# Kernel optimization log

Measured on AMD Instinct MI355X. Metric: run time of the kernel, lower is better.

The kernel has to match this reference:

```python
import jax, jax.numpy as jnp
import numpy as np

T, B, H, K, V, O, VS, DM = 128, 256, 128, 64, 128, 512, 3, 32


def _ln(x):
    m = jnp.mean(x, -1, keepdims=True)
    v = jnp.var(x, -1, keepdims=True)
    return (x - m) / jnp.sqrt(v + 1e-5)


def setup_inputs() -> dict:
    key = jax.random.key(0)
    ks = jax.random.split(key, 16)
    n = lambda k, shape, std=0.02: jax.random.normal(k, shape, jnp.float32) * std
    return {
        "obs": jax.random.randint(ks[0], (T, B), 0, O),
        "vel": jax.random.normal(ks[1], (T, B, VS), jnp.float32),
        "exploration": jax.random.uniform(ks[2], (T, B), dtype=jnp.float32),
        "hidden_init": n(ks[3], (1, H), 0.5),
        "embed_W": n(ks[4], (O, H)),
        "vel_W": n(ks[5], (H, VS)), "vel_b": jnp.zeros((H,), jnp.float32),
        "hyp_W1": n(ks[6], (DM, VS)), "hyp_b1": jnp.zeros((DM,), jnp.float32),
        "hyp_W2": n(ks[7], (H * H, DM), 0.001), "hyp_b2": jnp.zeros((H * H,), jnp.float32),
        "gate_W": n(ks[8], (H, 2 * H)), "gate_b": jnp.zeros((H,), jnp.float32),
        "pred_W": n(ks[9], (O, H)), "pred_b": jnp.zeros((O,), jnp.float32),
        "mem_W1": n(ks[10], (200, 3)), "mem_b1": jnp.zeros((200,), jnp.float32),
        "mem_W2": n(ks[11], (1, 200)), "mem_b2": jnp.zeros((1,), jnp.float32),
        "Wqk": n(ks[12], (K, H)), "Wv": n(ks[13], (V, H)),
    }


def reference(obs, vel, exploration, hidden_init, embed_W, vel_W, vel_b,
              hyp_W1, hyp_b1, hyp_W2, hyp_b2, gate_W, gate_b, pred_W, pred_b,
              mem_W1, mem_b1, mem_W2, mem_b2, Wqk, Wv):
    i_to_h_all = embed_W[obs]                                       # [T,B,H]
    vel_emb_all = jnp.einsum('tbv,hv->tbh', vel, vel_W) + vel_b      # [T,B,H]
    hyp_h = jax.nn.silu(jnp.einsum('tbv,dv->tbd', vel, hyp_W1) + hyp_b1)  # [T,B,DM]
    h0 = jnp.tanh(jnp.tile(hidden_init, (B, 1)))                     # [B,H]
    keys0 = jnp.zeros((T, B, K), jnp.float32)
    vals0 = jnp.zeros((T, B, V), jnp.float32)
    probs0 = jnp.zeros((T, B), jnp.float32)
    scale = 1.0 / np.sqrt(K).astype(np.float32)

    def step(carry, xs):
        hidden, keys, vals, probs = carry
        i, i_to_h, hyp_t, vemb_t, expl_t = xs
        # hypernet-generated per-sample transition matrix + path integration
        Tm = (hyp_t @ hyp_W2.T + hyp_b2).reshape(B, H, H)
        pi = jnp.einsum('bij,bj->bi', Tm, hidden) + vemb_t
        pi_pred = _ln(jnp.tanh(pi))
        # external-memory dot-product attention over stored (key, value) slots
        q = pi_pred @ Wqk.T                                          # [B,K]
        scores = jnp.einsum('bk,tbk->tb', q, keys) * scale           # [T,B]
        valid = jnp.arange(T)[:, None] < i
        attn = jax.nn.softmax(jnp.where(valid, scores, -1e9), axis=0)
        has_mem = (i > 0).astype(jnp.float32)
        mem_ret = jnp.einsum('tb,tbv->bv', attn * probs, vals) * has_mem
        mem = _ln(mem_ret)
        # sigmoid-gated RNN update between generative (pi) and input paths
        gate = jax.nn.sigmoid(jnp.concatenate([pi, i_to_h], -1) @ gate_W.T + gate_b)
        hidden_new = jnp.tanh(gate * pi + (1.0 - gate) * i_to_h)
        # EM model predicts from the retrieved + normalized memory
        logits = mem @ pred_W.T + pred_b                             # [B,O]
        # write decision MLP on [max inner prod, normalized position, exploration]
        max_ip = jnp.max(jnp.where(valid, scores, -1e9), axis=0) * has_mem
        pos = jnp.full((B,), 1.0, jnp.float32) * (i.astype(jnp.float32) / T)
        feat = jnp.stack([max_ip, pos, expl_t], -1)                  # [B,3]
        h1 = jax.nn.leaky_relu(feat @ mem_W1.T + mem_b1, 0.1)
        p_write = jax.nn.sigmoid(h1 @ mem_W2.T + mem_b2)[:, 0]
        keys = keys.at[i].set(hidden_new @ Wqk.T)
        vals = vals.at[i].set(hidden_new @ Wv.T)
        probs = probs.at[i].set(p_write)
        return (hidden_new, keys, vals, probs), (logits, hidden_new, pi, gate)

    xs = (jnp.arange(T), i_to_h_all, hyp_h, vel_emb_all, exploration)
    _, (logits, inf_h, gen, gating) = jax.lax.scan(step, (h0, keys0, vals0, probs0), xs)
    preds = jax.nn.softmax(logits, axis=-1)
    return preds, logits, inf_h, gen, gating
```

## Files before the change

kernel.cpp:

```cpp
#include <hip/hip_runtime.h>

#ifndef __has_builtin
#define __has_builtin(x) 0
#endif

#define DEV static __device__ __forceinline__

#define TT 128
#define BB 256
#define HH 128
#define KK 64
#define VV 128
#define OO 512
#define JBLK 132
#define KEXT (JBLK*32)

static const size_t PRED_OFF  = 0;
static const size_t LOGIT_OFF = (size_t)TT*BB*OO;
static const size_t INFH_OFF  = LOGIT_OFF + (size_t)TT*BB*OO;
static const size_t GEN_OFF   = INFH_OFF + (size_t)TT*BB*HH;
static const size_t GATE_OFF  = GEN_OFF + (size_t)TT*BB*HH;

DEV unsigned short f2bf(float x){
  unsigned int u = __float_as_uint(x);
  u = (u + 0x7fffu + ((u >> 16) & 1u)) >> 16;
  return (unsigned short)u;
}
DEV float bf2f(unsigned short v){ return __uint_as_float(((unsigned int)v) << 16); }

#if __has_builtin(__builtin_amdgcn_cvt_pk_f32_fp8)
#define FP8_FAST_DEC 1
typedef float floatx2 __attribute__((ext_vector_type(2)));
#endif

DEV float dec8_sw(unsigned int b){
  unsigned int s = b >> 7, e = (b >> 3) & 15u, m = b & 7u;
  float v = e ? ldexpf((float)(8u + m), (int)e - 10) : ldexpf((float)m, -9);
  return s ? -v : v;
}

DEV unsigned char enc8_sw(float x){
  unsigned int u = __float_as_uint(x);
  unsigned int s = (u >> 24) & 0x80u;
  int e = (int)((u >> 23) & 0xffu) - 127;
  unsigned int m = u & 0x7fffffu;
  if (((u >> 23) & 0xffu) == 0) return (unsigned char)s;
  if (e < -10) return (unsigned char)s;
  if (e >= -6) {
    unsigned int mant = m >> 20, rem = m & 0xfffffu;
    if (rem > 0x80000u || (rem == 0x80000u && (mant & 1u))) mant++;
    unsigned int ee = (unsigned int)(e + 7);
    if (mant == 8u) { mant = 0u; ee++; }
    if (ee >= 15u) return (unsigned char)(s | 0x7Eu);
    return (unsigned char)(s | (ee << 3) | mant);
  }
  unsigned int full = 0x800000u | m;
  int sh = 20 + (-6 - e);
  unsigned int mant = full >> sh;
  unsigned int rem  = full & ((1u << sh) - 1u);
  unsigned int halfv = 1u << (sh - 1);
  if (rem > halfv || (rem == halfv && (mant & 1u))) mant++;
  if (mant >= 8u) return (unsigned char)(s | (1u << 3));
  return (unsigned char)(s | mant);
}

DEV unsigned char enc8(float v){
#if __has_builtin(__builtin_amdgcn_cvt_pk_fp8_f32)
  int r = __builtin_amdgcn_cvt_pk_fp8_f32(v, v, 0, false);
  return (unsigned char)(r & 0xff);
#else
  return enc8_sw(v);
#endif
}

__global__ __launch_bounds__(256) void k_pack(const float* __restrict__ hW2,
                                              const float* __restrict__ hb2,
                                              unsigned char* __restrict__ w2p){
  int D = blockIdx.x * 256 + threadIdx.x;
  if (D >= KEXT * HH / 4) return;
  int bq = D & 3;
  int ig = (D >> 2) & 31;
  int h  = (D >> 7) & 1;
  int n  = (D >> 8) & 3;
  int j  = D >> 10;
  int i  = ig * 4 + n;
  unsigned int outw = 0;
  for (int c = 0; c < 4; ++c) {
    int bb = bq * 4 + c;
    int k = j * 32 + h * 16 + bb;
    float v;
    if (j < 128) v = hW2[((size_t)i * HH + j) * 32 + (k & 31)];
    else         v = hb2[(size_t)i * HH + (k - 4096)];
    v *= 1024.0f;
    outw |= ((unsigned int)enc8(v)) << (8 * c);
  }
  ((unsigned int*)w2p)[D] = outw;
}

struct ScanSmem {
  unsigned short gw[128 * 258];
  float part[16 * 128];
  float x[256];
  float pi[128];
  float i2h[128];
  float h[128];
  float hyp[32];
  float velWs[HH * 3];
  float velbs[HH];
  float hypW1s[32 * 3];
  float hypb1s[32];
  float gbs[HH];
  float vel3[4];
};

__global__ __launch_bounds__(512) void k_scan(
    const int* __restrict__ obs, const float* __restrict__ vel,
    const float* __restrict__ hinit, const float* __restrict__ embW,
    const float* __restrict__ velW, const float* __restrict__ velb,
    const float* __restrict__ hW1, const float* __restrict__ hb1,
    const float* __restrict__ gW, const float* __restrict__ gb,
    const unsigned char* __restrict__ w2p,
    float* __restrict__ out)
{
  extern __shared__ char smemraw[];
  ScanSmem* sm = (ScanSmem*)smemraw;
  const int tid = threadIdx.x;
  const int b = blockIdx.x;

  for (int idx = tid; idx < 128 * 256; idx += 512) {
    int i = idx >> 8, c = idx & 255;
    sm->gw[i * 258 + c] = f2bf(gW[i * 256 + c]);
  }
  for (int idx = tid; idx < HH * 3; idx += 512) sm->velWs[idx] = velW[idx];
  for (int idx = tid; idx < HH; idx += 512) { sm->velbs[idx] = velb[idx]; sm->gbs[idx] = gb[idx]; }
  for (int idx = tid; idx < 96; idx += 512) sm->hypW1s[idx] = hW1[idx];
  if (tid < 32) sm->hypb1s[tid] = hb1[tid];
  if (tid < 128) sm->h[tid] = tanhf(hinit[tid]);
  __syncthreads();

  const int ig = tid & 31;
  const int ks = tid >> 5;
  const int jbeg = ks * 8 + (ks < 4 ? ks : 4);
  const int jend = jbeg + 8 + (ks < 4 ? 1 : 0);

  for (int t = 0; t < TT; ++t) {
    if (tid < 3) sm->vel3[tid] = vel[((size_t)t * BB + b) * 3 + tid];
    if (tid >= 128 && tid < 256) {
      int j = tid - 128;
      sm->i2h[j] = embW[(size_t)obs[t * BB + b] * HH + j];
    }
    __syncthreads();
    if (tid < 32) {
      float a = sm->vel3[0] * sm->hypW1s[tid * 3] + sm->vel3[1] * sm->hypW1s[tid * 3 + 1]
              + sm->vel3[2] * sm->hypW1s[tid * 3 + 2] + sm->hypb1s[tid];
      sm->hyp[tid] = a / (1.0f + __expf(-a));
    }
    __syncthreads();

    float hypr[32];
    #pragma unroll
    for (int d = 0; d < 32; d += 4) {
      float4 q4 = *(const float4*)&sm->hyp[d];
      hypr[d] = q4.x; hypr[d + 1] = q4.y; hypr[d + 2] = q4.z; hypr[d + 3] = q4.w;
    }

    float acc0 = 0.f, acc1 = 0.f, acc2 = 0.f, acc3 = 0.f;
    for (int j = jbeg; j < jend; ++j) {
      float uj[32];
      if (j < 128) {
        float hj = sm->h[j];
        #pragma unroll
        for (int d = 0; d < 32; ++d) uj[d] = hj * hypr[d];
      } else {
        int base = (j - 128) * 32;
        #pragma unroll
        for (int d = 0; d < 32; d += 4) {
          float4 q4 = *(const float4*)&sm->h[base + d];
          uj[d] = q4.x; uj[d + 1] = q4.y; uj[d + 2] = q4.z; uj[d + 3] = q4.w;
        }
      }
      const unsigned char* pj = w2p + (size_t)j * 4096 + (size_t)ig * 16;
      #pragma unroll
      for (int n = 0; n < 4; ++n) {
        uint4 wa = *(const uint4*)(pj + (n * 2 + 0) * 512);
        uint4 wb = *(const uint4*)(pj + (n * 2 + 1) * 512);
        const unsigned int* wpa = (const unsigned int*)&wa;
        const unsigned int* wpb = (const unsigned int*)&wb;
        float s = 0.f;
        #pragma unroll
        for (int q = 0; q < 4; ++q) {
          unsigned int ww = wpa[q];
#if defined(FP8_FAST_DEC)
          floatx2 lo = __builtin_amdgcn_cvt_pk_f32_fp8((int)ww, false);
          floatx2 hi = __builtin_amdgcn_cvt_pk_f32_fp8((int)ww, true);
          s += lo[0]*uj[q*4+0] + lo[1]*uj[q*4+1] + hi[0]*uj[q*4+2] + hi[1]*uj[q*4+3];
#else
          s += dec8_sw(ww & 0xffu)        * uj[q*4+0];
          s += dec8_sw((ww >> 8) & 0xffu) * uj[q*4+1];
          s += dec8_sw((ww >> 16) & 0xffu)* uj[q*4+2];
          s += dec8_sw((ww >> 24) & 0xffu)* uj[q*4+3];
#endif
        }
        #pragma unroll
        for (int q = 0; q < 4; ++q) {
          unsigned int ww = wpb[q];
#if defined(FP8_FAST_DEC)
          floatx2 lo = __builtin_amdgcn_cvt_pk_f32_fp8((int)ww, false);
          floatx2 hi = __builtin_amdgcn_cvt_pk_f32_fp8((int)ww, true);
          s += lo[0]*uj[16+q*4+0] + lo[1]*uj[16+q*4+1] + hi[0]*uj[16+q*4+2] + hi[1]*uj[16+q*4+3];
#else
          s += dec8_sw(ww & 0xffu)        * uj[16+q*4+0];
          s += dec8_sw((ww >> 8) & 0xffu) * uj[16+q*4+1];
          s += dec8_sw((ww >> 16) & 0xffu)* uj[16+q*4+2];
          s += dec8_sw((ww >> 24) & 0xffu)* uj[16+q*4+3];
#endif
        }
        if (n == 0) acc0 += s; else if (n == 1) acc1 += s; else if (n == 2) acc2 += s; else acc3 += s;
      }
    }
    *(float4*)&sm->part[ks * 128 + ig * 4] = make_float4(acc0, acc1, acc2, acc3);
    __syncthreads();

    if (tid < 128) {
      float s = 0.f;
      #pragma unroll
      for (int q = 0; q < 16; ++q) s += sm->part[q * 128 + tid];
      s *= (1.0f / 1024.0f);
      s += sm->vel3[0] * sm->velWs[tid * 3] + sm->vel3[1] * sm->velWs[tid * 3 + 1]
         + sm->vel3[2] * sm->velWs[tid * 3 + 2] + sm->velbs[tid];
      sm->pi[tid] = s;
      sm->x[tid] = s;
      out[GEN_OFF + ((size_t)t * BB + b) * HH + tid] = s;
    } else if (tid < 256) {
      sm->x[tid] = sm->i2h[tid - 128];
    }
    __syncthreads();

    {
      int i = tid & 127, kq = tid >> 7;
      const unsigned short* gr = &sm->gw[i * 258 + kq * 64];
      const float* xr = &sm->x[kq * 64];
      float s = 0.f;
      #pragma unroll 16
      for (int c = 0; c < 64; ++c) s += bf2f(gr[c]) * xr[c];
      sm->part[kq * 128 + i] = s;
    }
    __syncthreads();

    if (tid < 128) {
      float z = sm->part[tid] + sm->part[128 + tid] + sm->part[256 + tid] + sm->part[384 + tid] + sm->gbs[tid];
      float g = 1.0f / (1.0f + __expf(-z));
      float hn = tanhf(g * sm->pi[tid] + (1.0f - g) * sm->i2h[tid]);
      out[GATE_OFF + ((size_t)t * BB + b) * HH + tid] = g;
      out[INFH_OFF + ((size_t)t * BB + b) * HH + tid] = hn;
      sm->h[tid] = hn;
    }
    __syncthreads();
  }
}

struct QkvSmem {
  float wqk[64 * 132];
  float wv[128 * 132];
  float pp[132];
  float hh[132];
  float red[4];
  float stats[2];
};

__global__ __launch_bounds__(256) void k_qkv(const float* __restrict__ out,
    const float* __restrict__ Wqk, const float* __restrict__ Wv,
    float* __restrict__ qbuf, unsigned short* __restrict__ keysBF,
    unsigned short* __restrict__ valsBF)
{
  extern __shared__ char smemraw[];
  QkvSmem* sm = (QkvSmem*)smemraw;
  const int tid = threadIdx.x, b = blockIdx.x;

  for (int idx = tid; idx < 64 * 128; idx += 256) { int o = idx >> 7, j = idx & 127; sm->wqk[o * 132 + j] = Wqk[idx]; }
  for (int idx = tid; idx < 128 * 128; idx += 256) { int o = idx >> 7, j = idx & 127; sm->wv[o * 132 + j] = Wv[idx]; }
  __syncthreads();

  for (int t = 0; t < TT; ++t) {
    if (tid < 128) {
      size_t base = ((size_t)t * BB + b) * HH + tid;
      sm->hh[tid] = out[INFH_OFF + base];
      sm->pp[tid] = tanhf(out[GEN_OFF + base]);
    }
    __syncthreads();
    if (tid < 128) {
      float v = sm->pp[tid];
      float s1 = v, s2 = v * v;
      #pragma unroll
      for (int off = 32; off; off >>= 1) { s1 += __shfl_down(s1, off); s2 += __shfl_down(s2, off); }
      if ((tid & 63) == 0) { sm->red[tid >> 6] = s1; sm->red[2 + (tid >> 6)] = s2; }
    }
    __syncthreads();
    if (tid == 0) {
      float s1 = sm->red[0] + sm->red[1], s2 = sm->red[2] + sm->red[3];
      float m = s1 * (1.0f / 128.0f);
      float var = s2 * (1.0f / 128.0f) - m * m;
      sm->stats[0] = m; sm->stats[1] = rsqrtf(var + 1e-5f);
    }
    __syncthreads();
    if (tid < 128) sm->pp[tid] = (sm->pp[tid] - sm->stats[0]) * sm->stats[1];
    __syncthreads();
    {
      int o = tid;
      if (o < 64) {
        const float* wr = &sm->wqk[o * 132];
        float s = 0.f;
        #pragma unroll 8
        for (int j = 0; j < 128; j += 4) {
          float4 xv = *(const float4*)&sm->pp[j];
          float4 w4 = *(const float4*)&wr[j];
          s += xv.x * w4.x + xv.y * w4.y + xv.z * w4.z + xv.w * w4.w;
        }
        qbuf[((size_t)t * BB + b) * KK + o] = s;
      } else if (o < 128) {
        int kk = o - 64;
        const float* wr = &sm->wqk[kk * 132];
        float s = 0.f;
        #pragma unroll 8
        for (int j = 0; j < 128; j += 4) {
          float4 xv = *(const float4*)&sm->hh[j];
          float4 w4 = *(const float4*)&wr[j];
          s += xv.x * w4.x + xv.y * w4.y + xv.z * w4.z + xv.w * w4.w;
        }
        keysBF[((size_t)t * BB + b) * KK + kk] = f2bf(s);
      } else {
        int vv = o - 128;
        const float* wr = &sm->wv[vv * 132];
        float s = 0.f;
        #pragma unroll 8
        for (int j = 0; j < 128; j += 4) {
          float4 xv = *(const float4*)&sm->hh[j];
          float4 w4 = *(const float4*)&wr[j];
          s += xv.x * w4.x + xv.y * w4.y + xv.z * w4.z + xv.w * w4.w;
        }
        valsBF[((size_t)t * BB + b) * VV + vv] = f2bf(s);
      }
    }
    __syncthreads();
  }
}

struct ScoresSmem { float q[128 * 68]; };

__global__ __launch_bounds__(128) void k_scores(const float* __restrict__ qbuf,
    const unsigned short* __restrict__ keysBF, const float* __restrict__ expl,
    const float* __restrict__ mW1, const float* __restrict__ mb1,
    const float* __restrict__ mW2, const float* __restrict__ mb2,
    float* __restrict__ Sg, float* __restrict__ probs)
{
  extern __shared__ char smemraw[];
  ScoresSmem* sm = (ScoresSmem*)smemraw;
  const int tid = threadIdx.x, b = blockIdx.x;

  for (int idx = tid; idx < 128 * 64; idx += 128) {
    int tq = idx >> 6, c = idx & 63;
    sm->q[tq * 68 + c] = qbuf[((size_t)tq * BB + b) * KK + c];
  }
  float kreg[64];
  {
    const uint4* kp = (const uint4*)&keysBF[((size_t)tid * BB + b) * KK];
    #pragma unroll
    for (int qq = 0; qq < 8; ++qq) {
      uint4 kv = kp[qq];
      const unsigned short* ku = (const unsigned short*)&kv;
      #pragma unroll
      for (int c = 0; c < 8; ++c) kreg[qq * 8 + c] = bf2f(ku[c]);
    }
  }
  __syncthreads();

  float* srow = &Sg[(size_t)b * TT * TT];
  for (int tq = 0; tq < TT; ++tq) {
    float s = 0.f;
    #pragma unroll
    for (int c = 0; c < 64; c += 4) {
      float4 qv = *(const float4*)&sm->q[tq * 68 + c];
      s += qv.x * kreg[c] + qv.y * kreg[c + 1] + qv.z * kreg[c + 2] + qv.w * kreg[c + 3];
    }
    srow[(size_t)tq * TT + tid] = s * 0.125f;
  }
  __syncthreads();

  {
    int tq = tid;
    const float* r = &srow[(size_t)tq * TT];
    float mx = -3.0e38f;
    for (int tk = 0; tk < tq; ++tk) mx = fmaxf(mx, r[tk]);
    float f0 = (tq > 0) ? mx : 0.0f;
    float f1 = (float)tq * (1.0f / 128.0f);
    float f2 = expl[(size_t)tq * BB + b];
    float a = 0.f;
    for (int u = 0; u < 200; ++u) {
      float h1 = mW1[u * 3] * f0 + mW1[u * 3 + 1] * f1 + mW1[u * 3 + 2] * f2 + mb1[u];
      h1 = (h1 > 0.f) ? h1 : 0.1f * h1;
      a += mW2[u] * h1;
    }
    float p = 1.0f / (1.0f + __expf(-(a + mb2[0])));
    probs[(size_t)b * TT + tq] = p;
  }
}

struct AttnSmem {
  float w[32 * 132];
  float mem[32 * 132];
  float pw[128 * 132];
};

__global__ __launch_bounds__(256) void k_attn(const float* __restrict__ Sg,
    const float* __restrict__ probs, const unsigned short* __restrict__ valsBF,
    const float* __restrict__ pW, const float* __restrict__ pb,
    float* __restrict__ out)
{
  extern __shared__ char smemraw[];
  AttnSmem* sm = (AttnSmem*)smemraw;
  const int tid = threadIdx.x;
  const int t = blockIdx.x >> 3, g = blockIdx.x & 7;
  const int bloc = tid >> 3, s8 = tid & 7;
  const int b = g * 32 + bloc;

  float acc[16];
  #pragma unroll
  for (int c = 0; c < 16; ++c) acc[c] = 0.f;

  float inv = 0.f;
  if (t > 0) {
    const float* srow = &Sg[((size_t)b * TT + t) * TT];
    float mx = -3.0e38f;
    for (int tk = s8; tk < t; tk += 8) mx = fmaxf(mx, srow[tk]);
    #pragma unroll
    for (int off = 4; off; off >>= 1) mx = fmaxf(mx, __shfl_xor(mx, off, 8));
    float es = 0.f;
    for (int tk = s8; tk < t; tk += 8) {
      float e = __expf(srow[tk] - mx);
      es += e;
      sm->w[bloc * 132 + tk] = e * probs[(size_t)b * TT + tk];
    }
    #pragma unroll
    for (int off = 4; off; off >>= 1) es += __shfl_xor(es, off, 8);
    inv = 1.0f / es;
  }
  __syncthreads();
  if (t > 0) {
    for (int tk = 0; tk < t; ++tk) {
      float wv = sm->w[bloc * 132 + tk] * inv;
      const uint4* vp = (const uint4*)&valsBF[((size_t)tk * BB + b) * VV + s8 * 16];
      uint4 v0 = vp[0], v1 = vp[1];
      const unsigned short* u0 = (const unsigned short*)&v0;
      const unsigned short* u1 = (const unsigned short*)&v1;
      #pragma unroll
      for (int c = 0; c < 8; ++c) acc[c] += wv * bf2f(u0[c]);
      #pragma unroll
      for (int c = 0; c < 8; ++c) acc[8 + c] += wv * bf2f(u1[c]);
    }
  }
  float s1 = 0.f, s2 = 0.f;
  #pragma unroll
  for (int c = 0; c < 16; ++c) { s1 += acc[c]; s2 += acc[c] * acc[c]; }
  #pragma unroll
  for (int off = 4; off; off >>= 1) { s1 += __shfl_xor(s1, off, 8); s2 += __shfl_xor(s2, off, 8); }
  float m = s1 * (1.0f / 128.0f);
  float var = s2 * (1.0f / 128.0f) - m * m;
  float sc = rsqrtf(var + 1e-5f);
  #pragma unroll
  for (int c = 0; c < 16; ++c) sm->mem[bloc * 132 + s8 * 16 + c] = (acc[c] - m) * sc;
  __syncthreads();

  const int og = tid >> 5, bl2 = tid & 31;
  const int b2 = g * 32 + bl2;
  for (int st = 0; st < 4; ++st) {
    for (int idx = tid; idx < 128 * 128; idx += 256) {
      int o = idx >> 7, i = idx & 127;
      sm->pw[o * 132 + i] = pW[((size_t)(st * 128 + o)) * HH + i];
    }
    __syncthreads();
    #pragma unroll
    for (int ob = 0; ob < 4; ++ob) {
      int oo = og * 16 + ob * 4;
      float a0 = pb[st * 128 + oo], a1 = pb[st * 128 + oo + 1];
      float a2 = pb[st * 128 + oo + 2], a3 = pb[st * 128 + oo + 3];
      for (int i = 0; i < 128; i += 4) {
        float4 mv = *(const float4*)&sm->mem[bl2 * 132 + i];
        float4 w0 = *(const float4*)&sm->pw[(oo + 0) * 132 + i];
        float4 w1 = *(const float4*)&sm->pw[(oo + 1) * 132 + i];
        float4 w2 = *(const float4*)&sm->pw[(oo + 2) * 132 + i];
        float4 w3 = *(const float4*)&sm->pw[(oo + 3) * 132 + i];
        a0 += mv.x * w0.x + mv.y * w0.y + mv.z * w0.z + mv.w * w0.w;
        a1 += mv.x * w1.x + mv.y * w1.y + mv.z * w1.z + mv.w * w1.w;
        a2 += mv.x * w2.x + mv.y * w2.y + mv.z * w2.z + mv.w * w2.w;
        a3 += mv.x * w3.x + mv.y * w3.y + mv.z * w3.z + mv.w * w3.w;
      }
      size_t base = LOGIT_OFF + ((size_t)t * BB + b2) * OO + st * 128 + oo;
      out[base] = a0; out[base + 1] = a1; out[base + 2] = a2; out[base + 3] = a3;
    }
    __syncthreads();
  }
  {
    const float* lrow = &out[LOGIT_OFF + ((size_t)t * BB + b) * OO];
    float mx = -3.0e38f;
    for (int o = s8; o < OO; o += 8) mx = fmaxf(mx, lrow[o]);
    #pragma unroll
    for (int off = 4; off; off >>= 1) mx = fmaxf(mx, __shfl_xor(mx, off, 8));
    float zs = 0.f;
    for (int o = s8; o < OO; o += 8) zs += __expf(lrow[o] - mx);
    #pragma unroll
    for (int off = 4; off; off >>= 1) zs += __shfl_xor(zs, off, 8);
    float zi = 1.0f / zs;
    float* prow = &out[PRED_OFF + ((size_t)t * BB + b) * OO];
    for (int o = s8; o < OO; o += 8) prow[o] = __expf(lrow[o] - mx) * zi;
  }
}

extern "C" void kernel_launch(void* const* d_in, const int* in_sizes, int n_in,
                              void* d_out, int out_size, void* d_ws, size_t ws_size,
                              hipStream_t stream) {
  (void)in_sizes; (void)n_in; (void)out_size; (void)ws_size;
  const int*   obs   = (const int*)d_in[0];
  const float* vel   = (const float*)d_in[1];
  const float* expl  = (const float*)d_in[2];
  const float* hinit = (const float*)d_in[3];
  const float* embW  = (const float*)d_in[4];
  const float* velW  = (const float*)d_in[5];
  const float* velb  = (const float*)d_in[6];
  const float* hW1   = (const float*)d_in[7];
  const float* hb1   = (const float*)d_in[8];
  const float* hW2   = (const float*)d_in[9];
  const float* hb2   = (const float*)d_in[10];
  const float* gW    = (const float*)d_in[11];
  const float* gb    = (const float*)d_in[12];
  const float* pW    = (const float*)d_in[13];
  const float* pb    = (const float*)d_in[14];
  const float* mW1   = (const float*)d_in[15];
  const float* mb1   = (const float*)d_in[16];
  const float* mW2   = (const float*)d_in[17];
  const float* mb2   = (const float*)d_in[18];
  const float* Wqk   = (const float*)d_in[19];
  const float* Wv    = (const float*)d_in[20];
  float* out = (float*)d_out;
  char* ws = (char*)d_ws;

  unsigned char*  w2p    = (unsigned char*)(ws + 0);
  float*          qbuf   = (float*)(ws + 1048576);
  unsigned short* keysBF = (unsigned short*)(ws + 9437184);
  unsigned short* valsBF = (unsigned short*)(ws + 13631488);
  float*          Sg     = (float*)(ws + 22020096);
  float*          probs  = (float*)(ws + 38797312);

  k_pack  <<<dim3(528),  dim3(256), 0,                  stream>>>(hW2, hb2, w2p);
  k_scan  <<<dim3(256),  dim3(512), sizeof(ScanSmem),   stream>>>(obs, vel, hinit, embW, velW, velb,
                                                                  hW1, hb1, gW, gb, w2p, out);
  k_qkv   <<<dim3(256),  dim3(256), sizeof(QkvSmem),    stream>>>(out, Wqk, Wv, qbuf, keysBF, valsBF);
  k_scores<<<dim3(256),  dim3(128), sizeof(ScoresSmem), stream>>>(qbuf, keysBF, expl, mW1, mb1, mW2, mb2,
                                                                  Sg, probs);
  k_attn  <<<dim3(1024), dim3(256), sizeof(AttnSmem),   stream>>>(Sg, probs, valsBF, pW, pb, out);
}
```

Baseline: 2.686 ms.

## Batch 16 samples per block in scan and use FP8 MFMA for hypernet and gate

The recurrent scan now processes 16 batch samples per workgroup (16 blocks instead of 256). Each step quantizes the per-sample activation vectors (h⊗hyp and [pi,i2h]) to FP8 and runs the hypernet transition and gate matmuls with 16x16x32 FP8 MFMA instructions. The gate weights are also pre-packed to FP8 in the pack kernel. This replaces per-sample scalar FP8 decode and FMA work with matrix-core work and amortizes weight reads across 16 samples. The cost is that only 16 CUs are busy, and activations quantized to FP8 may lose accuracy.

```diff
diff --git a/kernel.cpp b/kernel.cpp
--- a/kernel.cpp
+++ b/kernel.cpp
@@ -21,23 +21,14 @@
 static const size_t GEN_OFF   = INFH_OFF + (size_t)TT*BB*HH;
 static const size_t GATE_OFF  = GEN_OFF + (size_t)TT*BB*HH;
 
+typedef float f32x4 __attribute__((ext_vector_type(4)));
+
 DEV unsigned short f2bf(float x){
   unsigned int u = __float_as_uint(x);
   u = (u + 0x7fffu + ((u >> 16) & 1u)) >> 16;
   return (unsigned short)u;
 }
 DEV float bf2f(unsigned short v){ return __uint_as_float(((unsigned int)v) << 16); }
-
-#if __has_builtin(__builtin_amdgcn_cvt_pk_f32_fp8)
-#define FP8_FAST_DEC 1
-typedef float floatx2 __attribute__((ext_vector_type(2)));
-#endif
-
-DEV float dec8_sw(unsigned int b){
-  unsigned int s = b >> 7, e = (b >> 3) & 15u, m = b & 7u;
-  float v = e ? ldexpf((float)(8u + m), (int)e - 10) : ldexpf((float)m, -9);
-  return s ? -v : v;
-}
 
 DEV unsigned char enc8_sw(float x){
   unsigned int u = __float_as_uint(x);
@@ -73,187 +64,217 @@
 #endif
 }
 
+DEV unsigned int pack4_fp8(float a, float b, float c, float d){
+#if __has_builtin(__builtin_amdgcn_cvt_pk_fp8_f32)
+  int w = __builtin_amdgcn_cvt_pk_fp8_f32(a, b, 0, false);
+  w = __builtin_amdgcn_cvt_pk_fp8_f32(c, d, w, true);
+  return (unsigned int)w;
+#else
+  return (unsigned int)enc8_sw(a) | ((unsigned int)enc8_sw(b)<<8)
+       | ((unsigned int)enc8_sw(c)<<16) | ((unsigned int)enc8_sw(d)<<24);
+#endif
+}
+
+#define W2_DWORDS 135168
+#define GW_DWORDS 8192
 __global__ __launch_bounds__(256) void k_pack(const float* __restrict__ hW2,
                                               const float* __restrict__ hb2,
-                                              unsigned char* __restrict__ w2p){
+                                              const float* __restrict__ gW,
+                                              unsigned char* __restrict__ w2p,
+                                              unsigned char* __restrict__ gwp){
   int D = blockIdx.x * 256 + threadIdx.x;
-  if (D >= KEXT * HH / 4) return;
-  int bq = D & 3;
-  int ig = (D >> 2) & 31;
-  int h  = (D >> 7) & 1;
-  int n  = (D >> 8) & 3;
-  int j  = D >> 10;
-  int i  = ig * 4 + n;
-  unsigned int outw = 0;
-  for (int c = 0; c < 4; ++c) {
-    int bb = bq * 4 + c;
-    int k = j * 32 + h * 16 + bb;
-    float v;
-    if (j < 128) v = hW2[((size_t)i * HH + j) * 32 + (k & 31)];
-    else         v = hb2[(size_t)i * HH + (k - 4096)];
-    v *= 1024.0f;
-    outw |= ((unsigned int)enc8(v)) << (8 * c);
-  }
-  ((unsigned int*)w2p)[D] = outw;
-}
-
-struct ScanSmem {
-  unsigned short gw[128 * 258];
-  float part[16 * 128];
-  float x[256];
-  float pi[128];
-  float i2h[128];
-  float h[128];
-  float hyp[32];
-  float velWs[HH * 3];
-  float velbs[HH];
-  float hypW1s[32 * 3];
+  if (D < W2_DWORDS) {
+    int flat = D * 4;
+    int l  = (flat >> 3) & 63;
+    int w  = (flat >> 9) & 7;
+    int j  = flat >> 12;
+    int cb = flat & 7;
+    int i  = w*16 + (l & 15);
+    int db = ((l >> 4) << 3) + cb;
+    unsigned int outw = 0;
+    for (int cc = 0; cc < 4; ++cc) {
+      int d = db + cc;
+      float v;
+      if (j < 128) v = hW2[((size_t)i*128 + j)*32 + d];
+      else         v = hb2[(size_t)i*128 + (j-128)*32 + d];
+      outw |= ((unsigned int)enc8(v * 1024.0f)) << (8*cc);
+    }
+    ((unsigned int*)w2p)[D] = outw;
+  } else if (D < W2_DWORDS + GW_DWORDS) {
+    int Dg = D - W2_DWORDS;
+    int flat = Dg * 4;
+    int l  = (flat >> 3) & 63;
+    int w  = (flat >> 9) & 7;
+    int kc = flat >> 12;
+    int cb = flat & 7;
+    int i  = w*16 + (l & 15);
+    int k0 = kc*32 + ((l >> 4) << 3) + cb;
+    unsigned int outw = 0;
+    for (int cc = 0; cc < 4; ++cc)
+      outw |= ((unsigned int)enc8(gW[(size_t)i*256 + k0 + cc] * 64.0f)) << (8*cc);
+    ((unsigned int*)gwp)[Dg] = outw;
+  }
+}
+
+struct Scan2Smem {
+  unsigned long long U[JBLK*64];
+  unsigned long long GW[4096];
+  float h[128*17];
+  float pi[128*17];
+  float i2h[128*17];
+  float hyps[16*32];
+  float velg[64];
+  float velWs[384];
+  float velbs[128];
+  float gbs[128];
+  float hypW1s[96];
   float hypb1s[32];
-  float gbs[HH];
-  float vel3[4];
 };
 
-__global__ __launch_bounds__(512) void k_scan(
+__global__ __launch_bounds__(512) void k_scan2(
     const int* __restrict__ obs, const float* __restrict__ vel,
     const float* __restrict__ hinit, const float* __restrict__ embW,
     const float* __restrict__ velW, const float* __restrict__ velb,
     const float* __restrict__ hW1, const float* __restrict__ hb1,
-    const float* __restrict__ gW, const float* __restrict__ gb,
-    const unsigned char* __restrict__ w2p,
+    const float* __restrict__ gb,
+    const unsigned char* __restrict__ w2p, const unsigned char* __restrict__ gwp,
     float* __restrict__ out)
 {
   extern __shared__ char smemraw[];
-  ScanSmem* sm = (ScanSmem*)smemraw;
+  Scan2Smem* sm = (Scan2Smem*)smemraw;
   const int tid = threadIdx.x;
-  const int b = blockIdx.x;
-
-  for (int idx = tid; idx < 128 * 256; idx += 512) {
-    int i = idx >> 8, c = idx & 255;
-    sm->gw[i * 258 + c] = f2bf(gW[i * 256 + c]);
-  }
-  for (int idx = tid; idx < HH * 3; idx += 512) sm->velWs[idx] = velW[idx];
-  for (int idx = tid; idx < HH; idx += 512) { sm->velbs[idx] = velb[idx]; sm->gbs[idx] = gb[idx]; }
-  for (int idx = tid; idx < 96; idx += 512) sm->hypW1s[idx] = hW1[idx];
-  if (tid < 32) sm->hypb1s[tid] = hb1[tid];
-  if (tid < 128) sm->h[tid] = tanhf(hinit[tid]);
+  const int blk = blockIdx.x;
+  const int b0 = blk * 16;
+
+  const unsigned long long* gwu = (const unsigned long long*)gwp;
+  for (int idx = tid; idx < 4096; idx += 512) sm->GW[idx] = gwu[idx];
+  if (tid < 384) sm->velWs[tid] = velW[tid];
+  if (tid < 128) { sm->velbs[tid] = velb[tid]; sm->gbs[tid] = gb[tid]; }
+  if (tid < 96)  sm->hypW1s[tid] = hW1[tid];
+  if (tid < 32)  sm->hypb1s[tid] = hb1[tid];
+  if (tid < 128) {
+    float hv = tanhf(hinit[tid]);
+    #pragma unroll
+    for (int g = 0; g < 16; ++g) sm->h[tid*17+g] = hv;
+  }
   __syncthreads();
 
-  const int ig = tid & 31;
-  const int ks = tid >> 5;
-  const int jbeg = ks * 8 + (ks < 4 ? ks : 4);
-  const int jend = jbeg + 8 + (ks < 4 ? 1 : 0);
+  const int ln = tid & 63, wv = tid >> 6;
+  const int gg = tid & 15;
+  const int d0 = ((tid >> 4) & 3) << 3;
+  const unsigned long long* Au = (const unsigned long long*)w2p + (size_t)wv*64 + ln;
 
   for (int t = 0; t < TT; ++t) {
-    if (tid < 3) sm->vel3[tid] = vel[((size_t)t * BB + b) * 3 + tid];
-    if (tid >= 128 && tid < 256) {
-      int j = tid - 128;
-      sm->i2h[j] = embW[(size_t)obs[t * BB + b] * HH + j];
-    }
-    __syncthreads();
-    if (tid < 32) {
-      float a = sm->vel3[0] * sm->hypW1s[tid * 3] + sm->vel3[1] * sm->hypW1s[tid * 3 + 1]
-              + sm->vel3[2] * sm->hypW1s[tid * 3 + 2] + sm->hypb1s[tid];
-      sm->hyp[tid] = a / (1.0f + __expf(-a));
-    }
-    __syncthreads();
-
-    float hypr[32];
-    #pragma unroll
-    for (int d = 0; d < 32; d += 4) {
-      float4 q4 = *(const float4*)&sm->hyp[d];
-      hypr[d] = q4.x; hypr[d + 1] = q4.y; hypr[d + 2] = q4.z; hypr[d + 3] = q4.w;
-    }
-
-    float acc0 = 0.f, acc1 = 0.f, acc2 = 0.f, acc3 = 0.f;
-    for (int j = jbeg; j < jend; ++j) {
-      float uj[32];
-      if (j < 128) {
-        float hj = sm->h[j];
-        #pragma unroll
-        for (int d = 0; d < 32; ++d) uj[d] = hj * hypr[d];
-      } else {
-        int base = (j - 128) * 32;
-        #pragma unroll
-        for (int d = 0; d < 32; d += 4) {
-          float4 q4 = *(const float4*)&sm->h[base + d];
-          uj[d] = q4.x; uj[d + 1] = q4.y; uj[d + 2] = q4.z; uj[d + 3] = q4.w;
+    {
+      int g2 = tid >> 5, i0 = (tid & 31) << 2;
+      int ov = obs[t*BB + b0 + g2];
+      float4 e = *(const float4*)&embW[(size_t)ov*HH + i0];
+      sm->i2h[(i0+0)*17+g2] = e.x; sm->i2h[(i0+1)*17+g2] = e.y;
+      sm->i2h[(i0+2)*17+g2] = e.z; sm->i2h[(i0+3)*17+g2] = e.w;
+      int dh = tid & 31;
+      const float* vp = &vel[((size_t)t*BB + b0 + g2)*3];
+      float a = vp[0]*sm->hypW1s[dh*3+0] + vp[1]*sm->hypW1s[dh*3+1]
+              + vp[2]*sm->hypW1s[dh*3+2] + sm->hypb1s[dh];
+      sm->hyps[g2*32+dh] = a / (1.0f + __expf(-a));
+      if (tid < 48) sm->velg[(tid/3)*4 + tid%3] = vel[((size_t)t*BB + b0 + tid/3)*3 + tid%3];
+    }
+    __syncthreads();
+    {
+      float hyp8[8];
+      #pragma unroll
+      for (int c = 0; c < 8; ++c) hyp8[c] = sm->hyps[gg*32 + d0 + c];
+      #pragma unroll
+      for (int it = 0; it < 17; ++it) {
+        int j = wv + it*8;
+        if (j < JBLK) {
+          float u[8];
+          if (j < 128) {
+            float hv = sm->h[j*17+gg] * 32.0f;
+            #pragma unroll
+            for (int c = 0; c < 8; ++c) u[c] = hv * hyp8[c];
+          } else {
+            int jj = (j-128)*32 + d0;
+            #pragma unroll
+            for (int c = 0; c < 8; ++c) u[c] = sm->h[(jj+c)*17+gg] * 32.0f;
+          }
+          unsigned int w0 = pack4_fp8(u[0], u[1], u[2], u[3]);
+          unsigned int w1 = pack4_fp8(u[4], u[5], u[6], u[7]);
+          sm->U[j*64 + (tid & 63)] = ((unsigned long long)w1 << 32) | w0;
         }
       }
-      const unsigned char* pj = w2p + (size_t)j * 4096 + (size_t)ig * 16;
-      #pragma unroll
-      for (int n = 0; n < 4; ++n) {
-        uint4 wa = *(const uint4*)(pj + (n * 2 + 0) * 512);
-        uint4 wb = *(const uint4*)(pj + (n * 2 + 1) * 512);
-        const unsigned int* wpa = (const unsigned int*)&wa;
-        const unsigned int* wpb = (const unsigned int*)&wb;
-        float s = 0.f;
-        #pragma unroll
-        for (int q = 0; q < 4; ++q) {
-          unsigned int ww = wpa[q];
-#if defined(FP8_FAST_DEC)
-          floatx2 lo = __builtin_amdgcn_cvt_pk_f32_fp8((int)ww, false);
-          floatx2 hi = __builtin_amdgcn_cvt_pk_f32_fp8((int)ww, true);
-          s += lo[0]*uj[q*4+0] + lo[1]*uj[q*4+1] + hi[0]*uj[q*4+2] + hi[1]*uj[q*4+3];
-#else
-          s += dec8_sw(ww & 0xffu)        * uj[q*4+0];
-          s += dec8_sw((ww >> 8) & 0xffu) * uj[q*4+1];
-          s += dec8_sw((ww >> 16) & 0xffu)* uj[q*4+2];
-          s += dec8_sw((ww >> 24) & 0xffu)* uj[q*4+3];
-#endif
-        }
-        #pragma unroll
-        for (int q = 0; q < 4; ++q) {
-          unsigned int ww = wpb[q];
-#if defined(FP8_FAST_DEC)
-          floatx2 lo = __builtin_amdgcn_cvt_pk_f32_fp8((int)ww, false);
-          floatx2 hi = __builtin_amdgcn_cvt_pk_f32_fp8((int)ww, true);
-          s += lo[0]*uj[16+q*4+0] + lo[1]*uj[16+q*4+1] + hi[0]*uj[16+q*4+2] + hi[1]*uj[16+q*4+3];
-#else
-          s += dec8_sw(ww & 0xffu)        * uj[16+q*4+0];
-          s += dec8_sw((ww >> 8) & 0xffu) * uj[16+q*4+1];
-          s += dec8_sw((ww >> 16) & 0xffu)* uj[16+q*4+2];
-          s += dec8_sw((ww >> 24) & 0xffu)* uj[16+q*4+3];
-#endif
-        }
-        if (n == 0) acc0 += s; else if (n == 1) acc1 += s; else if (n == 2) acc2 += s; else acc3 += s;
-      }
-    }
-    *(float4*)&sm->part[ks * 128 + ig * 4] = make_float4(acc0, acc1, acc2, acc3);
-    __syncthreads();
-
-    if (tid < 128) {
-      float s = 0.f;
-      #pragma unroll
-      for (int q = 0; q < 16; ++q) s += sm->part[q * 128 + tid];
-      s *= (1.0f / 1024.0f);
-      s += sm->vel3[0] * sm->velWs[tid * 3] + sm->vel3[1] * sm->velWs[tid * 3 + 1]
-         + sm->vel3[2] * sm->velWs[tid * 3 + 2] + sm->velbs[tid];
-      sm->pi[tid] = s;
-      sm->x[tid] = s;
-      out[GEN_OFF + ((size_t)t * BB + b) * HH + tid] = s;
-    } else if (tid < 256) {
-      sm->x[tid] = sm->i2h[tid - 128];
-    }
-    __syncthreads();
-
-    {
-      int i = tid & 127, kq = tid >> 7;
-      const unsigned short* gr = &sm->gw[i * 258 + kq * 64];
-      const float* xr = &sm->x[kq * 64];
-      float s = 0.f;
-      #pragma unroll 16
-      for (int c = 0; c < 64; ++c) s += bf2f(gr[c]) * xr[c];
-      sm->part[kq * 128 + i] = s;
-    }
-    __syncthreads();
-
-    if (tid < 128) {
-      float z = sm->part[tid] + sm->part[128 + tid] + sm->part[256 + tid] + sm->part[384 + tid] + sm->gbs[tid];
-      float g = 1.0f / (1.0f + __expf(-z));
-      float hn = tanhf(g * sm->pi[tid] + (1.0f - g) * sm->i2h[tid]);
-      out[GATE_OFF + ((size_t)t * BB + b) * HH + tid] = g;
-      out[INFH_OFF + ((size_t)t * BB + b) * HH + tid] = hn;
-      sm->h[tid] = hn;
+    }
+    __syncthreads();
+    {
+      f32x4 a0 = {0.f,0.f,0.f,0.f}, a1 = a0, a2 = a0, a3 = a0;
+      #pragma unroll 3
+      for (int j4 = 0; j4 < JBLK; j4 += 4) {
+        long A0 = (long)Au[(size_t)(j4+0)*512]; long B0 = (long)sm->U[(j4+0)*64 + ln];
+        long A1 = (long)Au[(size_t)(j4+1)*512]; long B1 = (long)sm->U[(j4+1)*64 + ln];
+        long A2 = (long)Au[(size_t)(j4+2)*512]; long B2 = (long)sm->U[(j4+2)*64 + ln];
+        long A3 = (long)Au[(size_t)(j4+3)*512]; long B3 = (long)sm->U[(j4+3)*64 + ln];
+        a0 = __builtin_amdgcn_mfma_f32_16x16x32_fp8_fp8(A0, B0, a0, 0, 0, 0);
+        a1 = __builtin_amdgcn_mfma_f32_16x16x32_fp8_fp8(A1, B1, a1, 0, 0, 0);
+        a2 = __builtin_amdgcn_mfma_f32_16x16x32_fp8_fp8(A2, B2, a2, 0, 0, 0);
+        a3 = __builtin_amdgcn_mfma_f32_16x16x32_fp8_fp8(A3, B3, a3, 0, 0, 0);
+      }
+      f32x4 accT = (a0 + a1) + (a2 + a3);
+      #pragma unroll
+      for (int r = 0; r < 4; ++r) {
+        int i = wv*16 + ((ln>>4)<<2) + r, g = ln & 15;
+        float p = accT[r] * (1.0f/32768.0f)
+                + sm->velg[g*4+0]*sm->velWs[i*3+0] + sm->velg[g*4+1]*sm->velWs[i*3+1]
+                + sm->velg[g*4+2]*sm->velWs[i*3+2] + sm->velbs[i];
+        sm->pi[i*17+g] = p;
+      }
+    }
+    __syncthreads();
+    {
+      int kc = tid >> 6;
+      int k0 = kc*32 + d0;
+      float u[8];
+      #pragma unroll
+      for (int c = 0; c < 8; ++c) {
+        int k = k0 + c;
+        u[c] = (k < 128 ? sm->pi[k*17+gg] : sm->i2h[(k-128)*17+gg]) * 32.0f;
+      }
+      unsigned int w0 = pack4_fp8(u[0], u[1], u[2], u[3]);
+      unsigned int w1 = pack4_fp8(u[4], u[5], u[6], u[7]);
+      sm->U[kc*64 + (tid & 63)] = ((unsigned long long)w1 << 32) | w0;
+    }
+    __syncthreads();
+    {
+      f32x4 ga = {0.f,0.f,0.f,0.f};
+      #pragma unroll
+      for (int kc = 0; kc < 8; ++kc) {
+        long A = (long)sm->GW[(kc*8 + wv)*64 + ln];
+        long B = (long)sm->U[kc*64 + ln];
+        ga = __builtin_amdgcn_mfma_f32_16x16x32_fp8_fp8(A, B, ga, 0, 0, 0);
+      }
+      #pragma unroll
+      for (int r = 0; r < 4; ++r) {
+        int i = wv*16 + ((ln>>4)<<2) + r, g = ln & 15;
+        float z = ga[r] * (1.0f/2048.0f) + sm->gbs[i];
+        float gt = 1.0f / (1.0f + __expf(-z));
+        float pv = sm->pi[i*17+g], ih = sm->i2h[i*17+g];
+        float hn = tanhf(gt*pv + (1.0f - gt)*ih);
+        sm->h[i*17+g]   = hn;
+        sm->i2h[i*17+g] = gt;
+      }
+    }
+    __syncthreads();
+    {
+      int g2 = tid >> 5, i0 = (tid & 31) << 2;
+      size_t ob = ((size_t)t*BB + b0 + g2)*HH + i0;
+      float4 v;
+      v.x = sm->pi[(i0+0)*17+g2]; v.y = sm->pi[(i0+1)*17+g2];
+      v.z = sm->pi[(i0+2)*17+g2]; v.w = sm->pi[(i0+3)*17+g2];
+      *(float4*)&out[GEN_OFF + ob] = v;
+      v.x = sm->h[(i0+0)*17+g2];  v.y = sm->h[(i0+1)*17+g2];
+      v.z = sm->h[(i0+2)*17+g2];  v.w = sm->h[(i0+3)*17+g2];
+      *(float4*)&out[INFH_OFF + ob] = v;
+      v.x = sm->i2h[(i0+0)*17+g2]; v.y = sm->i2h[(i0+1)*17+g2];
+      v.z = sm->i2h[(i0+2)*17+g2]; v.w = sm->i2h[(i0+3)*17+g2];
+      *(float4*)&out[GATE_OFF + ob] = v;
     }
     __syncthreads();
   }
@@ -544,17 +565,18 @@
   char* ws = (char*)d_ws;
 
   unsigned char*  w2p    = (unsigned char*)(ws + 0);
+  unsigned char*  gwp    = (unsigned char*)(ws + 589824);
   float*          qbuf   = (float*)(ws + 1048576);
   unsigned short* keysBF = (unsigned short*)(ws + 9437184);
   unsigned short* valsBF = (unsigned short*)(ws + 13631488);
   float*          Sg     = (float*)(ws + 22020096);
   float*          probs  = (float*)(ws + 38797312);
 
-  k_pack  <<<dim3(528),  dim3(256), 0,                  stream>>>(hW2, hb2, w2p);
-  k_scan  <<<dim3(256),  dim3(512), sizeof(ScanSmem),   stream>>>(obs, vel, hinit, embW, velW, velb,
-                                                                  hW1, hb1, gW, gb, w2p, out);
-  k_qkv   <<<dim3(256),  dim3(256), sizeof(QkvSmem),    stream>>>(out, Wqk, Wv, qbuf, keysBF, valsBF);
-  k_scores<<<dim3(256),  dim3(128), sizeof(ScoresSmem), stream>>>(qbuf, keysBF, expl, mW1, mb1, mW2, mb2,
-                                                                  Sg, probs);
-  k_attn  <<<dim3(1024), dim3(256), sizeof(AttnSmem),   stream>>>(Sg, probs, valsBF, pW, pb, out);
-}
+  k_pack  <<<dim3(560),  dim3(256), 0,                   stream>>>(hW2, hb2, gW, w2p, gwp);
+  k_scan2 <<<dim3(16),   dim3(512), sizeof(Scan2Smem),   stream>>>(obs, vel, hinit, embW, velW, velb,
+                                                                   hW1, hb1, gb, w2p, gwp, out);
+  k_qkv   <<<dim3(256),  dim3(256), sizeof(QkvSmem),     stream>>>(out, Wqk, Wv, qbuf, keysBF, valsBF);
+  k_scores<<<dim3(256),  dim3(128), sizeof(ScoresSmem),  stream>>>(qbuf, keysBF, expl, mW1, mb1, mW2, mb2,
+                                                                   Sg, probs);
+  k_attn  <<<dim3(1024), dim3(256), sizeof(AttnSmem),    stream>>>(Sg, probs, valsBF, pW, pb, out);
+}
```

Measured after the change: 3.282 ms. 1.22x slower.
